# Optimization experiments

Measured on AMD Instinct MI355X. Metric: run time of the kernel, lower is better.

## Reference

```python
import jax, jax.numpy as jnp
import numpy as np

DIM = 1024
NUM_HEADS = 16
HEAD_DIM = DIM // NUM_HEADS
EPS = 1e-6


def setup_inputs() -> dict:
    key = jax.random.key(0)
    ks = jax.random.split(key, 9)
    B, N = 4, 4096
    scale = 1.0 / np.sqrt(DIM)
    inp = {
        "query": jax.random.normal(ks[0], (B, N, DIM), dtype=jnp.float32),
        "Wq": jax.random.normal(ks[1], (DIM, DIM), dtype=jnp.float32) * scale,
        "bq": jnp.zeros((DIM,), dtype=jnp.float32),
        "Wk": jax.random.normal(ks[2], (DIM, DIM), dtype=jnp.float32) * scale,
        "bk": jnp.zeros((DIM,), dtype=jnp.float32),
        "Wv": jax.random.normal(ks[3], (DIM, DIM), dtype=jnp.float32) * scale,
        "bv": jnp.zeros((DIM,), dtype=jnp.float32),
        "Wo": jax.random.normal(ks[4], (DIM, DIM), dtype=jnp.float32) * scale,
        "bo": jnp.zeros((DIM,), dtype=jnp.float32),
    }
    return inp


def _feature_map(x):
    # elu(x) + 1
    return jax.nn.elu(x) + 1.0


def reference(query, Wq, bq, Wk, bk, Wv, bv, Wo, bo):
    B, N, C = query.shape
    H, D = NUM_HEADS, HEAD_DIM
    # projections (torch Linear: x @ W.T + b)
    q = (query @ Wq.T + bq).reshape(B, N, H, D).transpose(0, 2, 1, 3)  # bhnd
    k = (query @ Wk.T + bk).reshape(B, N, H, D).transpose(0, 2, 1, 3)  # bhsd
    v = (query @ Wv.T + bv).reshape(B, N, H, D).transpose(0, 2, 1, 3)  # bhse
    q = _feature_map(q)
    k = _feature_map(k)
    # kv aggregation: [B,H,D,D]
    kv = jnp.einsum('bhsd,bhse->bhde', k, v)
    attn = jnp.einsum('bhqd,bhde->bhqe', q, kv)
    k_sum = k.sum(axis=2)  # bhd
    normalizer = jnp.einsum('bhqd,bhd->bhq', q, k_sum)[..., None] + EPS
    attn = attn / normalizer
    attn = attn.transpose(0, 2, 1, 3).reshape(B, N, C)
    # dropout p=0 -> identity
    return attn @ Wo.T + bo
```

## Files before the change

kernel.cpp:

```cpp
#include <hip/hip_runtime.h>

typedef __attribute__((ext_vector_type(8))) short short8;
typedef __attribute__((ext_vector_type(4))) float f32x4;

#define DEV static __device__ __forceinline__

DEV float bf2f(unsigned short b) { return __uint_as_float(((unsigned)b) << 16); }
DEV unsigned short f2bf(float f) {
  unsigned u = __float_as_uint(f);
  u += 0x7FFFu + ((u >> 16) & 1u);
  return (unsigned short)(u >> 16);
}

__global__ __launch_bounds__(256) void cast_bf16(const float* __restrict__ src,
                                                 unsigned short* __restrict__ dst, int n4) {
  int i = blockIdx.x * 256 + threadIdx.x;
  if (i >= n4) return;
  float4 f = ((const float4*)src)[i];
  unsigned lo = (unsigned)f2bf(f.x) | ((unsigned)f2bf(f.y) << 16);
  unsigned hi = (unsigned)f2bf(f.z) | ((unsigned)f2bf(f.w) << 16);
  ((uint2*)dst)[i] = make_uint2(lo, hi);
}

__global__ __launch_bounds__(256) void cast_w4(
    const float* __restrict__ w0, const float* __restrict__ w1,
    const float* __restrict__ w2, const float* __restrict__ w3,
    unsigned short* __restrict__ o0, unsigned short* __restrict__ o1,
    unsigned short* __restrict__ o2, unsigned short* __restrict__ o3) {
  const int which = blockIdx.y;
  const float* s = (which == 0) ? w0 : (which == 1) ? w1 : (which == 2) ? w2 : w3;
  unsigned short* d = (which == 0) ? o0 : (which == 1) ? o1 : (which == 2) ? o2 : o3;
  const int i = blockIdx.x * 256 + threadIdx.x;
  float4 f = ((const float4*)s)[i];
  unsigned lo = (unsigned)f2bf(f.x) | ((unsigned)f2bf(f.y) << 16);
  unsigned hi = (unsigned)f2bf(f.z) | ((unsigned)f2bf(f.w) << 16);
  ((uint2*)d)[i] = make_uint2(lo, hi);
}

DEV void stage_half(const unsigned short* __restrict__ g, int row0, int ldk, int kcol,
                    unsigned short* lbuf, int half, int wave, int lane) {
#pragma unroll
  for (int j = 0; j < 2; ++j) {
    const int row_lin = half * 128 + j * 64 + wave * 8 + (lane >> 3);
    const int k_src = (((lane & 7) ^ ((lane >> 3) & 7)) * 8);
    const unsigned short* src = g + (size_t)(row0 + row_lin) * ldk + kcol + k_src;
    unsigned short* dst = lbuf + half * 8192 + j * 4096 + wave * 512;
    __builtin_amdgcn_global_load_lds((const __attribute__((address_space(1))) void*)src,
                                     (__attribute__((address_space(3))) void*)dst, 16, 0, 0);
  }
}

#define BAR() do { asm volatile("" ::: "memory"); __builtin_amdgcn_s_barrier(); \
                   asm volatile("" ::: "memory"); } while (0)
#define LGKM0() asm volatile("s_waitcnt lgkmcnt(0)" ::: "memory")
#define VMC(n) asm volatile("s_waitcnt vmcnt(" #n ")" ::: "memory")

#define READ_A(qr) \
  _Pragma("unroll") for (int i4 = 0; i4 < 4; ++i4) \
  _Pragma("unroll") for (int ks = 0; ks < 2; ++ks) { \
    const int r_ = wrow + (qr) * 64 + i4 * 16 + fr; \
    a[i4][ks] = *(const short8*)(Abase + r_ * 128 + ((ks * 64 + kq16) ^ flip)); }

#define READ_B(qc) \
  _Pragma("unroll") for (int c2 = 0; c2 < 2; ++c2) \
  _Pragma("unroll") for (int ks = 0; ks < 2; ++ks) { \
    const int c_ = wcol + (qc) * 32 + c2 * 16 + fr; \
    b[qc][c2][ks] = *(const short8*)(Bbase + c_ * 128 + ((ks * 64 + kq16) ^ flip)); }

#define DO_MFMA(qr, qc) \
  _Pragma("unroll") for (int i4 = 0; i4 < 4; ++i4) \
  _Pragma("unroll") for (int c2 = 0; c2 < 2; ++c2) \
  _Pragma("unroll") for (int ks = 0; ks < 2; ++ks) \
    acc[(qr) * 4 + i4][(qc) * 2 + c2] = __builtin_amdgcn_mfma_f32_16x16x32_bf16( \
        a[i4][ks], b[qc][c2][ks], acc[(qr) * 4 + i4][(qc) * 2 + c2], 0, 0, 0);

template<int EPI>
__global__ __launch_bounds__(512, 2) void gemm256(
    const unsigned short* __restrict__ A, const unsigned short* __restrict__ Bt,
    const float* __restrict__ bias0, const float* __restrict__ bias1,
    const float* __restrict__ bias2,
    float* __restrict__ outF,
    unsigned short* __restrict__ oQ, unsigned short* __restrict__ oK,
    unsigned short* __restrict__ oV,
    int M, int N, int K)
{
  __shared__ alignas(16) unsigned short As[2][16384];
  __shared__ alignas(16) unsigned short Bs[2][16384];
  const int tid  = threadIdx.x;
  const int lane = tid & 63;
  const int wave = tid >> 6;
  const int wr = wave >> 2, wc = wave & 3;
  const int fr   = lane & 15;
  const int kq16 = (lane >> 4) * 16;
  const int flip = (fr & 7) << 4;
  const int nwg = gridDim.x, cpx = nwg >> 3, orig = blockIdx.x;
  const int logical = (orig & 7) * cpx + (orig >> 3);
  const int ntc = N >> 8;
  const int brow = (logical / ntc) << 8;
  const int bcol = (logical % ntc) << 8;
  const int NT = K >> 6;
  const int wrow = wr * 128, wcol = wc * 64;

  f32x4 acc[8][4] = {};
  short8 a[4][2], b[2][2][2];

  stage_half(A,  brow, K, 0, &As[0][0], 0, wave, lane);
  stage_half(A,  brow, K, 0, &As[0][0], 1, wave, lane);
  stage_half(Bt, bcol, K, 0, &Bs[0][0], 0, wave, lane);
  stage_half(Bt, bcol, K, 0, &Bs[0][0], 1, wave, lane);
  if (NT > 1) {
    stage_half(Bt, bcol, K, 64, &Bs[1][0], 0, wave, lane);
    stage_half(A,  brow, K, 64, &As[1][0], 0, wave, lane);
    VMC(4);
  } else {
    VMC(0);
  }
  BAR();

  for (int t = 0; t < NT; ++t) {
    const int cur = t & 1;
    const char* Abase = (const char*)&As[cur][0];
    const char* Bbase = (const char*)&Bs[cur][0];
    const int k1 = (t + 1) << 6, k2 = (t + 2) << 6;

    READ_A(0)
    READ_B(0)
    if (t < NT - 1) stage_half(Bt, bcol, K, k1, &Bs[cur ^ 1][0], 1, wave, lane);
    BAR(); LGKM0();
    __builtin_amdgcn_s_setprio(1);
    DO_MFMA(0, 0)
    __builtin_amdgcn_s_setprio(0);
    BAR();

    READ_B(1)
    if (t < NT - 1) stage_half(A, brow, K, k1, &As[cur ^ 1][0], 1, wave, lane);
    BAR(); LGKM0();
    __builtin_amdgcn_s_setprio(1);
    DO_MFMA(0, 1)
    __builtin_amdgcn_s_setprio(0);
    BAR();

    READ_A(1)
    if (t < NT - 2) stage_half(Bt, bcol, K, k2, &Bs[cur][0], 0, wave, lane);
    BAR(); LGKM0();
    __builtin_amdgcn_s_setprio(1);
    DO_MFMA(1, 0)
    __builtin_amdgcn_s_setprio(0);
    BAR();

    if (t < NT - 2) stage_half(A, brow, K, k2, &As[cur][0], 0, wave, lane);
    BAR();
    __builtin_amdgcn_s_setprio(1);
    DO_MFMA(1, 1)
    __builtin_amdgcn_s_setprio(0);
    if (t < NT - 2)      { VMC(4); }
    else if (t < NT - 1) { VMC(0); }
    BAR();
  }

  const int l4 = (lane >> 4) * 4;
#pragma unroll
  for (int rg = 0; rg < 8; ++rg) {
    const int row0 = brow + wrow + rg * 16 + l4;
#pragma unroll
    for (int cg = 0; cg < 4; ++cg) {
      const int col = bcol + wcol + cg * 16 + fr;
      if (EPI == 1) {
        const float bb = bias0[col];
#pragma unroll
        for (int q = 0; q < 4; ++q)
          outF[(size_t)(row0 + q) * N + col] = acc[rg][cg][q] + bb;
      } else {
        const int sel = col >> 10;
        const int o = col & 1023;
        const float* bp = (sel == 0) ? bias0 : (sel == 1) ? bias1 : bias2;
        unsigned short* dstp = (sel == 0) ? oQ : (sel == 1) ? oK : oV;
        const float bb = bp[o];
#pragma unroll
        for (int q = 0; q < 4; ++q) {
          float val = acc[rg][cg][q] + bb;
          if (sel < 2) val = (val > 0.f) ? (val + 1.f) : __expf(val);
          dstp[(size_t)(row0 + q) * 1024 + o] = f2bf(val);
        }
      }
    }
  }
}

__global__ __launch_bounds__(256) void kv_agg(
    const unsigned short* __restrict__ kbuf, const unsigned short* __restrict__ vbuf,
    float* __restrict__ part_kv, float* __restrict__ part_ks)
{
  __shared__ alignas(16) unsigned short Ksm[16 * 64];
  __shared__ alignas(16) unsigned short Vsm[16 * 64];
  const int blk = blockIdx.x;
  const int bh = blk >> 4, chunk = blk & 15;
  const int bb = bh >> 4, h = bh & 15;
  const int t = threadIdx.x;
  const int d0 = (t >> 4) * 4;
  const int e0 = (t & 15) * 4;
  const int ls = (t & 127) >> 3;
  const int lc = (t & 7) * 8;
  float acc[4][4] = {};
  float ks[4] = {0.f, 0.f, 0.f, 0.f};
  const int rb = bb * 4096 + chunk * 256;
  for (int ss = 0; ss < 256; ss += 16) {
    __syncthreads();
    const size_t ga = (size_t)(rb + ss + ls) * 1024 + h * 64 + lc;
    if (t < 128) *(uint4*)&Ksm[ls * 64 + lc] = *(const uint4*)&kbuf[ga];
    else         *(uint4*)&Vsm[ls * 64 + lc] = *(const uint4*)&vbuf[ga];
    __syncthreads();
#pragma unroll
    for (int i = 0; i < 16; ++i) {
      const unsigned ku0 = *(const unsigned*)&Ksm[i * 64 + d0];
      const unsigned ku1 = *(const unsigned*)&Ksm[i * 64 + d0 + 2];
      const unsigned vu0 = *(const unsigned*)&Vsm[i * 64 + e0];
      const unsigned vu1 = *(const unsigned*)&Vsm[i * 64 + e0 + 2];
      const float kk0 = __uint_as_float(ku0 << 16), kk1 = __uint_as_float(ku0 & 0xFFFF0000u);
      const float kk2 = __uint_as_float(ku1 << 16), kk3 = __uint_as_float(ku1 & 0xFFFF0000u);
      const float vv0 = __uint_as_float(vu0 << 16), vv1 = __uint_as_float(vu0 & 0xFFFF0000u);
      const float vv2 = __uint_as_float(vu1 << 16), vv3 = __uint_as_float(vu1 & 0xFFFF0000u);
      ks[0] += kk0; ks[1] += kk1; ks[2] += kk2; ks[3] += kk3;
      acc[0][0] += kk0 * vv0; acc[0][1] += kk0 * vv1; acc[0][2] += kk0 * vv2; acc[0][3] += kk0 * vv3;
      acc[1][0] += kk1 * vv0; acc[1][1] += kk1 * vv1; acc[1][2] += kk1 * vv2; acc[1][3] += kk1 * vv3;
      acc[2][0] += kk2 * vv0; acc[2][1] += kk2 * vv1; acc[2][2] += kk2 * vv2; acc[2][3] += kk2 * vv3;
      acc[3][0] += kk3 * vv0; acc[3][1] += kk3 * vv1; acc[3][2] += kk3 * vv2; acc[3][3] += kk3 * vv3;
    }
  }
#pragma unroll
  for (int r = 0; r < 4; ++r)
    *(float4*)&part_kv[((size_t)blk * 64 + d0 + r) * 64 + e0] =
        make_float4(acc[r][0], acc[r][1], acc[r][2], acc[r][3]);
  if ((t & 15) == 0) {
#pragma unroll
    for (int r = 0; r < 4; ++r) part_ks[blk * 64 + d0 + r] = ks[r];
  }
}

__global__ __launch_bounds__(256) void kv_reduce(
    const float* __restrict__ part_kv, const float* __restrict__ part_ks,
    unsigned short* __restrict__ kvTb, float* __restrict__ ksf)
{
  const int bh = blockIdx.x;
  const int t = threadIdx.x;
#pragma unroll
  for (int i = 0; i < 16; ++i) {
    const int lin = i * 256 + t;
    float s = 0.f;
#pragma unroll
    for (int c = 0; c < 16; ++c) s += part_kv[((size_t)(bh * 16 + c)) * 4096 + lin];
    const int d = lin >> 6, e = lin & 63;
    kvTb[(size_t)bh * 4096 + e * 64 + d] = f2bf(s);
  }
  if (t < 64) {
    float s = 0.f;
#pragma unroll
    for (int c = 0; c < 16; ++c) s += part_ks[(bh * 16 + c) * 64 + t];
    ksf[bh * 64 + t] = s;
  }
}

__global__ __launch_bounds__(256) void attn_mfma(
    const unsigned short* __restrict__ qbuf,
    const unsigned short* __restrict__ kvTb,
    const float* __restrict__ ksf,
    unsigned short* __restrict__ attnb)
{
  __shared__ alignas(16) unsigned short kvs[64 * 64];
  __shared__ float ks_lds[64];
  __shared__ float inv_lds[256];
  const int blk = blockIdx.x;
  const int bh = blk >> 4, ntile = blk & 15;
  const int bb = bh >> 4, h = bh & 15;
  const int t = threadIdx.x;
  const int lane = t & 63, w = t >> 6;
  const int fr = lane & 15, kg = lane >> 4;

  {
    const unsigned short* src = kvTb + (size_t)bh * 4096;
#pragma unroll
    for (int c = 0; c < 2; ++c) {
      const int slot = t * 2 + c;
      const int e = slot >> 3, sl = slot & 7;
      short8 v = *(const short8*)&src[e * 64 + sl * 8];
      *(short8*)&kvs[e * 64 + (sl ^ (e & 7)) * 8] = v;
    }
    if (t < 64) ks_lds[t] = ksf[bh * 64 + t];
  }

  const size_t gq = (size_t)bb * 4096 + ntile * 256 + w * 64;
  short8 a[4][2];
#pragma unroll
  for (int rg = 0; rg < 4; ++rg)
#pragma unroll
    for (int ks = 0; ks < 2; ++ks)
      a[rg][ks] = *(const short8*)&qbuf[(gq + rg * 16 + fr) * 1024 + h * 64 + ks * 32 + kg * 8];
  __syncthreads();

#pragma unroll
  for (int rg = 0; rg < 4; ++rg) {
    float p = 0.f;
#pragma unroll
    for (int ks = 0; ks < 2; ++ks)
#pragma unroll
      for (int j = 0; j < 8; ++j)
        p += bf2f(((const unsigned short*)&a[rg][ks])[j]) * ks_lds[ks * 32 + kg * 8 + j];
    p += __shfl_xor(p, 16);
    p += __shfl_xor(p, 32);
    if (kg == 0) inv_lds[w * 64 + rg * 16 + fr] = 1.f / (p + 1e-6f);
  }

  const int flip = (fr & 7) << 4;
  const int kq16 = kg * 16;
  short8 bf[4][2];
#pragma unroll
  for (int cg = 0; cg < 4; ++cg)
#pragma unroll
    for (int ks = 0; ks < 2; ++ks)
      bf[cg][ks] = *(const short8*)((const char*)kvs + (cg * 16 + fr) * 128 + ((ks * 64 + kq16) ^ flip));
  f32x4 acc[4][4] = {};
#pragma unroll
  for (int rg = 0; rg < 4; ++rg)
#pragma unroll
    for (int cg = 0; cg < 4; ++cg)
#pragma unroll
      for (int ks = 0; ks < 2; ++ks)
        acc[rg][cg] = __builtin_amdgcn_mfma_f32_16x16x32_bf16(a[rg][ks], bf[cg][ks], acc[rg][cg], 0, 0, 0);

  __syncthreads();

#pragma unroll
  for (int rg = 0; rg < 4; ++rg)
#pragma unroll
    for (int cg = 0; cg < 4; ++cg)
#pragma unroll
      for (int q = 0; q < 4; ++q) {
        const int r = rg * 16 + kg * 4 + q;
        const float iv = inv_lds[w * 64 + r];
        attnb[(gq + r) * 1024 + h * 64 + cg * 16 + fr] = f2bf(acc[rg][cg][q] * iv);
      }
}

extern "C" void kernel_launch(void* const* d_in, const int* in_sizes, int n_in,
                              void* d_out, int out_size, void* d_ws, size_t ws_size,
                              hipStream_t stream)
{
  const float* query = (const float*)d_in[0];
  const float* Wq = (const float*)d_in[1];
  const float* bq = (const float*)d_in[2];
  const float* Wk = (const float*)d_in[3];
  const float* bk = (const float*)d_in[4];
  const float* Wv = (const float*)d_in[5];
  const float* bv = (const float*)d_in[6];
  const float* Wo = (const float*)d_in[7];
  const float* bo = (const float*)d_in[8];
  float* out = (float*)d_out;

  const int M = in_sizes[0] / 1024;

  char* ws = (char*)d_ws;
  unsigned short* qbf   = (unsigned short*)(ws);
  unsigned short* attnb = (unsigned short*)(ws);
  unsigned short* wqkv  = (unsigned short*)(ws + 33554432);
  unsigned short* wobf  = (unsigned short*)(ws + 39845888);
  unsigned short* phiq  = (unsigned short*)(ws + 41943040);
  unsigned short* phik  = (unsigned short*)(ws + 75497472);
  unsigned short* vbf   = (unsigned short*)(ws + 109051904);
  float*          pkv   = (float*)(ws + 142606336);
  float*          pks   = (float*)(ws + 159383552);
  unsigned short* kvTb  = (unsigned short*)(ws + 159645696);
  float*          ksf   = (float*)(ws + 160169984);

  cast_bf16<<<(M * 1024 / 4 + 255) / 256, 256, 0, stream>>>(query, qbf, M * 1024 / 4);
  cast_w4<<<dim3(1024, 4), 256, 0, stream>>>(Wq, Wk, Wv, Wo,
                                             wqkv, wqkv + 1048576, wqkv + 2097152, wobf);

  gemm256<0><<<dim3((M / 256) * (3072 / 256)), 512, 0, stream>>>(
      qbf, wqkv, bq, bk, bv, nullptr, phiq, phik, vbf, M, 3072, 1024);

  kv_agg<<<1024, 256, 0, stream>>>(phik, vbf, pkv, pks);
  kv_reduce<<<64, 256, 0, stream>>>(pkv, pks, kvTb, ksf);
  attn_mfma<<<1024, 256, 0, stream>>>(phiq, kvTb, ksf, attnb);

  gemm256<1><<<dim3((M / 256) * (1024 / 256)), 512, 0, stream>>>(
      attnb, wobf, bo, nullptr, nullptr, out, nullptr, nullptr, nullptr, M, 1024, 1024);
}
```

Before: 242.3 us.

## Restructure GEMM main loop into triple-buffered 32-wide K tiles

```diff
diff --git a/kernel.cpp b/kernel.cpp
--- a/kernel.cpp
+++ b/kernel.cpp
@@ -37,14 +37,16 @@
   ((uint2*)d)[i] = make_uint2(lo, hi);
 }
 
-DEV void stage_half(const unsigned short* __restrict__ g, int row0, int ldk, int kcol,
-                    unsigned short* lbuf, int half, int wave, int lane) {
+
+DEV void stage32(const unsigned short* __restrict__ g, int row0, int ldk, int kcol,
+                 unsigned short* lbuf, int wave, int lane) {
 #pragma unroll
   for (int j = 0; j < 2; ++j) {
-    const int row_lin = half * 128 + j * 64 + wave * 8 + (lane >> 3);
-    const int k_src = (((lane & 7) ^ ((lane >> 3) & 7)) * 8);
-    const unsigned short* src = g + (size_t)(row0 + row_lin) * ldk + kcol + k_src;
-    unsigned short* dst = lbuf + half * 8192 + j * 4096 + wave * 512;
+    const int rbase = j * 128 + wave * 16;
+    const int row = rbase + (lane >> 2);
+    const int k_src = (((lane & 3) ^ ((lane >> 2) & 3)) * 8);
+    const unsigned short* src = g + (size_t)(row0 + row) * ldk + kcol + k_src;
+    unsigned short* dst = lbuf + rbase * 32;
     __builtin_amdgcn_global_load_lds((const __attribute__((address_space(1))) void*)src,
                                      (__attribute__((address_space(3))) void*)dst, 16, 0, 0);
   }
@@ -52,27 +54,35 @@
 
 #define BAR() do { asm volatile("" ::: "memory"); __builtin_amdgcn_s_barrier(); \
                    asm volatile("" ::: "memory"); } while (0)
-#define LGKM0() asm volatile("s_waitcnt lgkmcnt(0)" ::: "memory")
 #define VMC(n) asm volatile("s_waitcnt vmcnt(" #n ")" ::: "memory")
 
-#define READ_A(qr) \
-  _Pragma("unroll") for (int i4 = 0; i4 < 4; ++i4) \
-  _Pragma("unroll") for (int ks = 0; ks < 2; ++ks) { \
-    const int r_ = wrow + (qr) * 64 + i4 * 16 + fr; \
-    a[i4][ks] = *(const short8*)(Abase + r_ * 128 + ((ks * 64 + kq16) ^ flip)); }
-
-#define READ_B(qc) \
-  _Pragma("unroll") for (int c2 = 0; c2 < 2; ++c2) \
-  _Pragma("unroll") for (int ks = 0; ks < 2; ++ks) { \
-    const int c_ = wcol + (qc) * 32 + c2 * 16 + fr; \
-    b[qc][c2][ks] = *(const short8*)(Bbase + c_ * 128 + ((ks * 64 + kq16) ^ flip)); }
-
-#define DO_MFMA(qr, qc) \
-  _Pragma("unroll") for (int i4 = 0; i4 < 4; ++i4) \
-  _Pragma("unroll") for (int c2 = 0; c2 < 2; ++c2) \
-  _Pragma("unroll") for (int ks = 0; ks < 2; ++ks) \
-    acc[(qr) * 4 + i4][(qc) * 2 + c2] = __builtin_amdgcn_mfma_f32_16x16x32_bf16( \
-        a[i4][ks], b[qc][c2][ks], acc[(qr) * 4 + i4][(qc) * 2 + c2], 0, 0, 0);
+#define READ_A32(base) \
+  _Pragma("unroll") for (int rg = 0; rg < 8; ++rg) \
+    a[rg] = *(const short8*)((const char*)(base) + (wrow + rg * 16 + fr) * 64 + (kg16 ^ flip2));
+
+#define READ_B32(base) \
+  _Pragma("unroll") for (int cg = 0; cg < 4; ++cg) \
+    bb[cg] = *(const short8*)((const char*)(base) + (wcol + cg * 16 + fr) * 64 + (kg16 ^ flip2));
+
+#define MFMA32() \
+  _Pragma("unroll") for (int rg = 0; rg < 8; ++rg) \
+  _Pragma("unroll") for (int cg = 0; cg < 4; ++cg) \
+    acc[rg][cg] = __builtin_amdgcn_mfma_f32_16x16x32_bf16(a[rg], bb[cg], acc[rg][cg], 0, 0, 0);
+
+#define TB(j, BI) do { \
+  const int j_ = (j); \
+  const bool h2 = (j_ + 2 < NT), h1 = (j_ + 1 < NT); \
+  if (h2) { \
+    stage32(A,  brow, K, (j_ + 2) * 32, &As[(BI + 2) % 3][0], wave, lane); \
+    stage32(Bt, bcol, K, (j_ + 2) * 32, &Bs[(BI + 2) % 3][0], wave, lane); \
+  } \
+  READ_A32(&As[BI][0]) \
+  READ_B32(&Bs[BI][0]) \
+  MFMA32() \
+  if (h2)      { VMC(4); } \
+  else if (h1) { VMC(0); } \
+  BAR(); \
+} while (0)
 
 template<int EPI>
 __global__ __launch_bounds__(512, 2) void gemm256(
@@ -84,78 +94,37 @@
     unsigned short* __restrict__ oV,
     int M, int N, int K)
 {
-  __shared__ alignas(16) unsigned short As[2][16384];
-  __shared__ alignas(16) unsigned short Bs[2][16384];
+  __shared__ alignas(16) unsigned short As[3][8192];
+  __shared__ alignas(16) unsigned short Bs[3][8192];
   const int tid  = threadIdx.x;
   const int lane = tid & 63;
   const int wave = tid >> 6;
   const int wr = wave >> 2, wc = wave & 3;
   const int fr   = lane & 15;
-  const int kq16 = (lane >> 4) * 16;
-  const int flip = (fr & 7) << 4;
+  const int kg16 = (lane >> 4) * 16;
+  const int flip2 = (fr & 3) << 4;
   const int nwg = gridDim.x, cpx = nwg >> 3, orig = blockIdx.x;
   const int logical = (orig & 7) * cpx + (orig >> 3);
   const int ntc = N >> 8;
   const int brow = (logical / ntc) << 8;
   const int bcol = (logical % ntc) << 8;
-  const int NT = K >> 6;
+  const int NT = K >> 5;
   const int wrow = wr * 128, wcol = wc * 64;
 
   f32x4 acc[8][4] = {};
-  short8 a[4][2], b[2][2][2];
-
-  stage_half(A,  brow, K, 0, &As[0][0], 0, wave, lane);
-  stage_half(A,  brow, K, 0, &As[0][0], 1, wave, lane);
-  stage_half(Bt, bcol, K, 0, &Bs[0][0], 0, wave, lane);
-  stage_half(Bt, bcol, K, 0, &Bs[0][0], 1, wave, lane);
-  if (NT > 1) {
-    stage_half(Bt, bcol, K, 64, &Bs[1][0], 0, wave, lane);
-    stage_half(A,  brow, K, 64, &As[1][0], 0, wave, lane);
-    VMC(4);
-  } else {
-    VMC(0);
-  }
+  short8 a[8], bb[4];
+
+  stage32(A,  brow, K, 0,  &As[0][0], wave, lane);
+  stage32(Bt, bcol, K, 0,  &Bs[0][0], wave, lane);
+  stage32(A,  brow, K, 32, &As[1][0], wave, lane);
+  stage32(Bt, bcol, K, 32, &Bs[1][0], wave, lane);
+  VMC(4);
   BAR();
 
-  for (int t = 0; t < NT; ++t) {
-    const int cur = t & 1;
-    const char* Abase = (const char*)&As[cur][0];
-    const char* Bbase = (const char*)&Bs[cur][0];
-    const int k1 = (t + 1) << 6, k2 = (t + 2) << 6;
-
-    READ_A(0)
-    READ_B(0)
-    if (t < NT - 1) stage_half(Bt, bcol, K, k1, &Bs[cur ^ 1][0], 1, wave, lane);
-    BAR(); LGKM0();
-    __builtin_amdgcn_s_setprio(1);
-    DO_MFMA(0, 0)
-    __builtin_amdgcn_s_setprio(0);
-    BAR();
-
-    READ_B(1)
-    if (t < NT - 1) stage_half(A, brow, K, k1, &As[cur ^ 1][0], 1, wave, lane);
-    BAR(); LGKM0();
-    __builtin_amdgcn_s_setprio(1);
-    DO_MFMA(0, 1)
-    __builtin_amdgcn_s_setprio(0);
-    BAR();
-
-    READ_A(1)
-    if (t < NT - 2) stage_half(Bt, bcol, K, k2, &Bs[cur][0], 0, wave, lane);
-    BAR(); LGKM0();
-    __builtin_amdgcn_s_setprio(1);
-    DO_MFMA(1, 0)
-    __builtin_amdgcn_s_setprio(0);
-    BAR();
-
-    if (t < NT - 2) stage_half(A, brow, K, k2, &As[cur][0], 0, wave, lane);
-    BAR();
-    __builtin_amdgcn_s_setprio(1);
-    DO_MFMA(1, 1)
-    __builtin_amdgcn_s_setprio(0);
-    if (t < NT - 2)      { VMC(4); }
-    else if (t < NT - 1) { VMC(0); }
-    BAR();
+  for (int j = 0; j < NT; j += 3) {
+    TB(j, 0);
+    if (j + 1 < NT) TB(j + 1, 1);
+    if (j + 2 < NT) TB(j + 2, 2);
   }
 
   const int l4 = (lane >> 4) * 4;
@@ -166,19 +135,19 @@
     for (int cg = 0; cg < 4; ++cg) {
       const int col = bcol + wcol + cg * 16 + fr;
       if (EPI == 1) {
-        const float bb = bias0[col];
+        const float bv_ = bias0[col];
 #pragma unroll
         for (int q = 0; q < 4; ++q)
-          outF[(size_t)(row0 + q) * N + col] = acc[rg][cg][q] + bb;
+          outF[(size_t)(row0 + q) * N + col] = acc[rg][cg][q] + bv_;
       } else {
         const int sel = col >> 10;
         const int o = col & 1023;
         const float* bp = (sel == 0) ? bias0 : (sel == 1) ? bias1 : bias2;
         unsigned short* dstp = (sel == 0) ? oQ : (sel == 1) ? oK : oV;
-        const float bb = bp[o];
+        const float bv_ = bp[o];
 #pragma unroll
         for (int q = 0; q < 4; ++q) {
-          float val = acc[rg][cg][q] + bb;
+          float val = acc[rg][cg][q] + bv_;
           if (sel < 2) val = (val > 0.f) ? (val + 1.f) : __expf(val);
           dstp[(size_t)(row0 + q) * 1024 + o] = f2bf(val);
         }
```

After: 267.3 us. 10.3% more time.

## Prefetch next LDS fragments during MFMA and merge cast kernels

Applied to the files above, without the earlier changes.

```diff
diff --git a/kernel.cpp b/kernel.cpp
--- a/kernel.cpp
+++ b/kernel.cpp
@@ -12,30 +12,31 @@
   return (unsigned short)(u >> 16);
 }
 
-__global__ __launch_bounds__(256) void cast_bf16(const float* __restrict__ src,
-                                                 unsigned short* __restrict__ dst, int n4) {
-  int i = blockIdx.x * 256 + threadIdx.x;
-  if (i >= n4) return;
-  float4 f = ((const float4*)src)[i];
-  unsigned lo = (unsigned)f2bf(f.x) | ((unsigned)f2bf(f.y) << 16);
-  unsigned hi = (unsigned)f2bf(f.z) | ((unsigned)f2bf(f.w) << 16);
-  ((uint2*)dst)[i] = make_uint2(lo, hi);
-}
-
-__global__ __launch_bounds__(256) void cast_w4(
+__global__ __launch_bounds__(256) void cast_all(
+    const float* __restrict__ q,
     const float* __restrict__ w0, const float* __restrict__ w1,
     const float* __restrict__ w2, const float* __restrict__ w3,
+    unsigned short* __restrict__ oq,
     unsigned short* __restrict__ o0, unsigned short* __restrict__ o1,
     unsigned short* __restrict__ o2, unsigned short* __restrict__ o3) {
-  const int which = blockIdx.y;
-  const float* s = (which == 0) ? w0 : (which == 1) ? w1 : (which == 2) ? w2 : w3;
-  unsigned short* d = (which == 0) ? o0 : (which == 1) ? o1 : (which == 2) ? o2 : o3;
-  const int i = blockIdx.x * 256 + threadIdx.x;
+  const int b = blockIdx.x;
+  const float* s;
+  unsigned short* d;
+  int i;
+  if (b < 16384) {
+    s = q; d = oq; i = b * 256 + threadIdx.x;
+  } else {
+    const int wsel = (b - 16384) >> 10, wb = (b - 16384) & 1023;
+    s = (wsel == 0) ? w0 : (wsel == 1) ? w1 : (wsel == 2) ? w2 : w3;
+    d = (wsel == 0) ? o0 : (wsel == 1) ? o1 : (wsel == 2) ? o2 : o3;
+    i = wb * 256 + threadIdx.x;
+  }
   float4 f = ((const float4*)s)[i];
   unsigned lo = (unsigned)f2bf(f.x) | ((unsigned)f2bf(f.y) << 16);
   unsigned hi = (unsigned)f2bf(f.z) | ((unsigned)f2bf(f.w) << 16);
   ((uint2*)d)[i] = make_uint2(lo, hi);
 }
+
 
 DEV void stage_half(const unsigned short* __restrict__ g, int row0, int ldk, int kcol,
                     unsigned short* lbuf, int half, int wave, int lane) {
@@ -54,25 +55,26 @@
                    asm volatile("" ::: "memory"); } while (0)
 #define LGKM0() asm volatile("s_waitcnt lgkmcnt(0)" ::: "memory")
 #define VMC(n) asm volatile("s_waitcnt vmcnt(" #n ")" ::: "memory")
-
-#define READ_A(qr) \
+#define SCHED0() __builtin_amdgcn_sched_barrier(0)
+
+#define READ_Aset(dst, qr, base) \
   _Pragma("unroll") for (int i4 = 0; i4 < 4; ++i4) \
   _Pragma("unroll") for (int ks = 0; ks < 2; ++ks) { \
     const int r_ = wrow + (qr) * 64 + i4 * 16 + fr; \
-    a[i4][ks] = *(const short8*)(Abase + r_ * 128 + ((ks * 64 + kq16) ^ flip)); }
-
-#define READ_B(qc) \
+    dst[i4][ks] = *(const short8*)((base) + r_ * 128 + ((ks * 64 + kq16) ^ flip)); }
+
+#define READ_Bset(dst, qc, base) \
   _Pragma("unroll") for (int c2 = 0; c2 < 2; ++c2) \
   _Pragma("unroll") for (int ks = 0; ks < 2; ++ks) { \
     const int c_ = wcol + (qc) * 32 + c2 * 16 + fr; \
-    b[qc][c2][ks] = *(const short8*)(Bbase + c_ * 128 + ((ks * 64 + kq16) ^ flip)); }
-
-#define DO_MFMA(qr, qc) \
+    dst[c2][ks] = *(const short8*)((base) + c_ * 128 + ((ks * 64 + kq16) ^ flip)); }
+
+#define MMQ(qr, qc, A_, B_) \
   _Pragma("unroll") for (int i4 = 0; i4 < 4; ++i4) \
   _Pragma("unroll") for (int c2 = 0; c2 < 2; ++c2) \
   _Pragma("unroll") for (int ks = 0; ks < 2; ++ks) \
     acc[(qr) * 4 + i4][(qc) * 2 + c2] = __builtin_amdgcn_mfma_f32_16x16x32_bf16( \
-        a[i4][ks], b[qc][c2][ks], acc[(qr) * 4 + i4][(qc) * 2 + c2], 0, 0, 0);
+        A_[i4][ks], B_[c2][ks], acc[(qr) * 4 + i4][(qc) * 2 + c2], 0, 0, 0);
 
 template<int EPI>
 __global__ __launch_bounds__(512, 2) void gemm256(
@@ -102,7 +104,7 @@
   const int wrow = wr * 128, wcol = wc * 64;
 
   f32x4 acc[8][4] = {};
-  short8 a[4][2], b[2][2][2];
+  short8 a[4][2], b0[2][2], b1[2][2];
 
   stage_half(A,  brow, K, 0, &As[0][0], 0, wave, lane);
   stage_half(A,  brow, K, 0, &As[0][0], 1, wave, lane);
@@ -116,45 +118,52 @@
     VMC(0);
   }
   BAR();
+  READ_Aset(a, 0, (const char*)&As[0][0])
+  READ_Bset(b0, 0, (const char*)&Bs[0][0])
 
   for (int t = 0; t < NT; ++t) {
     const int cur = t & 1;
-    const char* Abase = (const char*)&As[cur][0];
-    const char* Bbase = (const char*)&Bs[cur][0];
+    const char* Ac = (const char*)&As[cur][0];
+    const char* Bc = (const char*)&Bs[cur][0];
+    const char* An = (const char*)&As[cur ^ 1][0];
+    const char* Bn = (const char*)&Bs[cur ^ 1][0];
     const int k1 = (t + 1) << 6, k2 = (t + 2) << 6;
-
-    READ_A(0)
-    READ_B(0)
-    if (t < NT - 1) stage_half(Bt, bcol, K, k1, &Bs[cur ^ 1][0], 1, wave, lane);
+    const bool h1 = t < NT - 1, h2 = t < NT - 2;
+
+    if (h1) stage_half(Bt, bcol, K, k1, &Bs[cur ^ 1][0], 1, wave, lane);
     BAR(); LGKM0();
     __builtin_amdgcn_s_setprio(1);
-    DO_MFMA(0, 0)
+    MMQ(0, 0, a, b0)
     __builtin_amdgcn_s_setprio(0);
-    BAR();
-
-    READ_B(1)
-    if (t < NT - 1) stage_half(A, brow, K, k1, &As[cur ^ 1][0], 1, wave, lane);
+    SCHED0();
+    READ_Bset(b1, 1, Bc)
+    BAR();
+
+    if (h1) stage_half(A, brow, K, k1, &As[cur ^ 1][0], 1, wave, lane);
     BAR(); LGKM0();
     __builtin_amdgcn_s_setprio(1);
-    DO_MFMA(0, 1)
+    MMQ(0, 1, a, b1)
     __builtin_amdgcn_s_setprio(0);
-    BAR();
-
-    READ_A(1)
-    if (t < NT - 2) stage_half(Bt, bcol, K, k2, &Bs[cur][0], 0, wave, lane);
+    SCHED0();
+    READ_Aset(a, 1, Ac)
+    BAR();
+
+    if (h2) stage_half(Bt, bcol, K, k2, &Bs[cur][0], 0, wave, lane);
     BAR(); LGKM0();
     __builtin_amdgcn_s_setprio(1);
-    DO_MFMA(1, 0)
+    MMQ(1, 0, a, b0)
     __builtin_amdgcn_s_setprio(0);
     BAR();
 
-    if (t < NT - 2) stage_half(A, brow, K, k2, &As[cur][0], 0, wave, lane);
+    if (h2) stage_half(A, brow, K, k2, &As[cur][0], 0, wave, lane);
     BAR();
     __builtin_amdgcn_s_setprio(1);
-    DO_MFMA(1, 1)
+    MMQ(1, 1, a, b1)
     __builtin_amdgcn_s_setprio(0);
-    if (t < NT - 2)      { VMC(4); }
-    else if (t < NT - 1) { VMC(0); }
+    if (h2)      { VMC(4); }
+    else if (h1) { VMC(0); }
+    SCHED0();
+    if (h1) { READ_Aset(a, 0, An) READ_Bset(b0, 0, Bn) }
     BAR();
   }
 
@@ -371,9 +380,8 @@
   unsigned short* kvTb  = (unsigned short*)(ws + 159645696);
   float*          ksf   = (float*)(ws + 160169984);
 
-  cast_bf16<<<(M * 1024 / 4 + 255) / 256, 256, 0, stream>>>(query, qbf, M * 1024 / 4);
-  cast_w4<<<dim3(1024, 4), 256, 0, stream>>>(Wq, Wk, Wv, Wo,
-                                             wqkv, wqkv + 1048576, wqkv + 2097152, wobf);
+  cast_all<<<20480, 256, 0, stream>>>(query, Wq, Wk, Wv, Wo,
+                                      qbf, wqkv, wqkv + 1048576, wqkv + 2097152, wobf);
 
   gemm256<0><<<dim3((M / 256) * (3072 / 256)), 512, 0, stream>>>(
       qbf, wqkv, bq, bk, bv, nullptr, phiq, phik, vbf, M, 3072, 1024);
```

Measured after the change: 249.2 us. +2.9%, slower.
